# Kernel optimization log

Hardware: AMD Instinct MI355X
Metric: run time of the kernel (lower is better)

## Reference

```python
import jax, jax.numpy as jnp
import numpy as np

FEA, DK, H = 768, 64, 12
B, L = 4, 1024
MASK_VAL = -2**15 + 1  # matches torch masked_fill constant


def setup_inputs() -> dict:
    key = jax.random.key(0)
    ks = jax.random.split(key, 16)
    d = {
        'qx': jax.random.normal(ks[0], (B, L, FEA), jnp.float32),
        'kx': jax.random.normal(ks[1], (B, L, FEA), jnp.float32),
        'vx': jax.random.normal(ks[2], (B, L, FEA), jnp.float32),
        'preScores': jax.random.normal(ks[3], (B, H, L, L), jnp.float32),
        'maskPAD': jax.random.randint(ks[4], (B, L, L), 0, 2, jnp.int32),
    }
    s = 1.0 / np.sqrt(FEA)
    d['WQ_w'] = jax.random.normal(ks[5], (H * DK, FEA), jnp.float32) * s
    d['WQ_b'] = jnp.zeros((H * DK,), jnp.float32)
    d['WK_w'] = jax.random.normal(ks[6], (H * DK, FEA), jnp.float32) * s
    d['WK_b'] = jnp.zeros((H * DK,), jnp.float32)
    d['WV_w'] = jax.random.normal(ks[7], (H * DK, FEA), jnp.float32) * s
    d['WV_b'] = jnp.zeros((H * DK,), jnp.float32)
    d['WO_w'] = jax.random.normal(ks[8], (FEA, H * DK), jnp.float32) * s
    d['WO_b'] = jnp.zeros((FEA,), jnp.float32)
    return d


def reference(qx, kx, vx, preScores, maskPAD,
              WQ_w, WQ_b, WK_w, WK_b, WV_w, WV_b, WO_w, WO_b):
    b, l, c = qx.shape
    # projections -> (B, H, L, dk)
    q = (qx @ WQ_w.T + WQ_b).reshape(b, l, H, DK).transpose(0, 2, 1, 3)
    k = (kx @ WK_w.T + WK_b).reshape(b, l, H, DK).transpose(0, 2, 1, 3)
    v = (vx @ WV_w.T + WV_b).reshape(b, l, H, DK).transpose(0, 2, 1, 3)
    scores = jnp.einsum('bhqd,bhkd->bhqk', q, k) / np.sqrt(DK)
    scores = scores + preScores  # RealFormer residual scores
    scores = jnp.where((maskPAD == 0)[:, None, :, :], jnp.float32(MASK_VAL), scores)
    alpha = jax.nn.softmax(scores, axis=3)  # dropout p=0 (eval/deterministic)
    z = jnp.einsum('bhqk,bhkd->bhqd', alpha, v)
    z = z.transpose(0, 2, 1, 3).reshape(b, l, H * DK)
    z = z @ WO_w.T + WO_b
    return z, scores
```

## Files before the change

### kernel.cpp

```cpp
#include <hip/hip_runtime.h>
#include <hip/hip_bf16.h>

#define B_ 4
#define L_ 1024
#define H_ 12
#define DK_ 64
#define FEA_ 768
#define MASKV (-32767.0f)

typedef __attribute__((ext_vector_type(8))) short bf16x8;
typedef __attribute__((ext_vector_type(4))) short s16x4;
typedef __attribute__((ext_vector_type(4))) float f32x4;
typedef unsigned int u32;

__device__ inline short f2bf(float x) {
  __hip_bfloat16 h = __float2bfloat16(x);
  return __builtin_bit_cast(short, h);
}

#define SZX  (4 * 1024 * 768)
#define SZW  (768 * 768)

__global__ __launch_bounds__(256) void k_cvt(
    const float* __restrict__ qx, const float* __restrict__ kx,
    const float* __restrict__ vx,
    const float* __restrict__ Wq, const float* __restrict__ Wk,
    const float* __restrict__ Wv,
    unsigned short* __restrict__ dst)
{
  const size_t SZX4 = SZX / 4, SZW4 = SZW / 4;
  const size_t total4 = 3 * SZX4 + 3 * SZW4;
  for (size_t i4 = (size_t)blockIdx.x * 256 + threadIdx.x; i4 < total4;
       i4 += (size_t)gridDim.x * 256) {
    const float* src; size_t o4; size_t db;
    if (i4 < SZX4)               { src = qx; o4 = i4;               db = 0; }
    else if (i4 < 2 * SZX4)      { src = kx; o4 = i4 - SZX4;        db = (size_t)SZX; }
    else if (i4 < 3 * SZX4)      { src = vx; o4 = i4 - 2 * SZX4;    db = 2 * (size_t)SZX; }
    else if (i4 < 3 * SZX4 + SZW4)     { src = Wq; o4 = i4 - 3 * SZX4;            db = 3 * (size_t)SZX; }
    else if (i4 < 3 * SZX4 + 2 * SZW4) { src = Wk; o4 = i4 - 3 * SZX4 - SZW4;     db = 3 * (size_t)SZX + SZW; }
    else                               { src = Wv; o4 = i4 - 3 * SZX4 - 2 * SZW4; db = 3 * (size_t)SZX + 2 * (size_t)SZW; }
    float4 v = ((const float4*)src)[o4];
    s16x4 r = {f2bf(v.x), f2bf(v.y), f2bf(v.z), f2bf(v.w)};
    *(s16x4*)(dst + db + o4 * 4) = r;
  }
}

__global__ __launch_bounds__(256) void k_cvt2(
    const float* __restrict__ Wo, unsigned short* __restrict__ dst)
{
  size_t i4 = (size_t)blockIdx.x * 256 + threadIdx.x;
  if (i4 < (size_t)SZW / 4) {
    float4 v = ((const float4*)Wo)[i4];
    s16x4 r = {f2bf(v.x), f2bf(v.y), f2bf(v.z), f2bf(v.w)};
    *(s16x4*)(dst + i4 * 4) = r;
  }
}

__global__ __launch_bounds__(256) void k_proj(
    const unsigned short* __restrict__ qxb, const unsigned short* __restrict__ kxb,
    const unsigned short* __restrict__ vxb,
    const unsigned short* __restrict__ Wqb, const unsigned short* __restrict__ Wkb,
    const unsigned short* __restrict__ Wvb,
    const float* __restrict__ bq, const float* __restrict__ bk,
    const float* __restrict__ bv,
    unsigned short* __restrict__ Qb, unsigned short* __restrict__ Kb,
    unsigned short* __restrict__ Vt)
{
  __shared__ short lA[2][64 * 64];
  __shared__ short lB[2][64 * 64];

  const int which = blockIdx.z;
  const unsigned short* __restrict__ Ab = (which == 0) ? qxb : (which == 1) ? kxb : vxb;
  const unsigned short* __restrict__ Wb = (which == 0) ? Wqb : (which == 1) ? Wkb : Wvb;
  const float* __restrict__ bias = (which == 0) ? bq : (which == 1) ? bk : bv;

  const int tid = threadIdx.x;
  const int lane = tid & 63;
  const int wid = tid >> 6;
  const int wr = wid >> 1, wc = wid & 1;
  const int m0 = blockIdx.x * 64;
  const int n0 = blockIdx.y * 64;
  const int g = lane >> 4, qc = lane & 15;
  const int srow = lane >> 3;
  const int spos = lane & 7;

#define PSTAGE(buf, ktof)                                                      \
  {                                                                            \
    _Pragma("unroll")                                                          \
    for (int i_ = 0; i_ < 2; i_++) {                                           \
      int r0_ = wid * 16 + i_ * 8;                                             \
      int row_ = r0_ + srow;                                                   \
      int cs_ = spos ^ (row_ & 7);                                             \
      __builtin_amdgcn_global_load_lds(                                        \
          (const __attribute__((address_space(1))) u32*)(Ab +                  \
              (size_t)(m0 + row_) * FEA_ + (ktof) + cs_ * 8),                  \
          (__attribute__((address_space(3))) u32*)&lA[buf][r0_ * 64],          \
          16, 0, 0);                                                           \
      __builtin_amdgcn_global_load_lds(                                        \
          (const __attribute__((address_space(1))) u32*)(Wb +                  \
              (size_t)(n0 + row_) * FEA_ + (ktof) + cs_ * 8),                  \
          (__attribute__((address_space(3))) u32*)&lB[buf][r0_ * 64],          \
          16, 0, 0);                                                           \
    }                                                                          \
  }

  f32x4 acc[2][2];
#pragma unroll
  for (int i = 0; i < 2; i++)
#pragma unroll
    for (int j = 0; j < 2; j++) acc[i][j] = f32x4{0.f, 0.f, 0.f, 0.f};

  PSTAGE(0, 0);
  asm volatile("s_waitcnt vmcnt(0)" ::: "memory");
  __builtin_amdgcn_s_barrier();

  for (int kt = 0; kt < 12; kt++) {
    const int cur = kt & 1, nxt = cur ^ 1;
    if (kt < 11) PSTAGE(nxt, (kt + 1) * 64);
    __builtin_amdgcn_sched_barrier(0);
    __builtin_amdgcn_s_setprio(1);
#pragma unroll
    for (int s = 0; s < 2; s++) {
      bf16x8 af[2], bfr[2];
#pragma unroll
      for (int i = 0; i < 2; i++) {
        int ar = wr * 32 + i * 16 + qc;
        af[i] = *(const bf16x8*)&lA[cur][ar * 64 + (((s * 4 + g) ^ (ar & 7)) << 3)];
        int br = wc * 32 + i * 16 + qc;
        bfr[i] = *(const bf16x8*)&lB[cur][br * 64 + (((s * 4 + g) ^ (br & 7)) << 3)];
      }
#pragma unroll
      for (int i = 0; i < 2; i++)
#pragma unroll
        for (int j = 0; j < 2; j++)
          acc[i][j] = __builtin_amdgcn_mfma_f32_16x16x32_bf16(af[i], bfr[j], acc[i][j], 0, 0, 0);
    }
    __builtin_amdgcn_s_setprio(0);
    asm volatile("s_waitcnt vmcnt(0)" ::: "memory");
    __builtin_amdgcn_s_barrier();
  }

  const int cn0 = n0 + wc * 32;
  float bv2[2];
#pragma unroll
  for (int j = 0; j < 2; j++) bv2[j] = bias[cn0 + j * 16 + qc];

#pragma unroll
  for (int i = 0; i < 2; i++) {
    int m = m0 + wr * 32 + i * 16 + g * 4;
    int bb = m >> 10;
    int l = m & 1023;
#pragma unroll
    for (int j = 0; j < 2; j++) {
      int n = cn0 + j * 16 + qc;
      int hh = n >> 6, d = n & 63;
      if (which == 2) {
        s16x4 vv = {f2bf(acc[i][j][0] + bv2[j]), f2bf(acc[i][j][1] + bv2[j]),
                    f2bf(acc[i][j][2] + bv2[j]), f2bf(acc[i][j][3] + bv2[j])};
        *(s16x4*)&Vt[(((size_t)bb * H_ + hh) * DK_ + d) * L_ + l] = vv;
      } else {
#pragma unroll
        for (int r = 0; r < 4; r++) {
          unsigned short v = (unsigned short)f2bf(acc[i][j][r] + bv2[j]);
          if (which == 0) {
            Qb[(((size_t)bb * H_ + hh) * L_ + (l + r)) * DK_ + d] = v;
          } else {
            Kb[(((size_t)bb * H_ + hh) * L_ + (l + r)) * DK_ + d] = v;
          }
        }
      }
    }
  }
#undef PSTAGE
}

__global__ __launch_bounds__(256, 3) void k_attn(
    const unsigned short* __restrict__ Qb, const unsigned short* __restrict__ Kb,
    const unsigned short* __restrict__ Vt,
    const float* __restrict__ preScores, const int* __restrict__ maskPAD,
    float* __restrict__ scoresOut, unsigned short* __restrict__ zp)
{
  __shared__ short lK[2][64 * 64];
  __shared__ short lV[2][64 * 64];
  __shared__ float lU[4][1120];

  const int tid = threadIdx.x, lane = tid & 63, wid = tid >> 6;
  const int bi = blockIdx.x;
  const int slot = bi >> 3;
  const int bh_i = (bi & 7) * 6 + (slot >> 4);
  const int qt = slot & 15;
  const int b = bh_i / H_;
  const int h = bh_i % H_;
  const int q0 = qt * 64;
  const int g = lane >> 4, qr = lane & 15;
  const int qrow = q0 + wid * 16 + qr;
  const int rhi = lane >> 4, klo = lane & 15;
  const int rowCg = q0 + wid * 16 + rhi;

  const size_t bh = (size_t)b * H_ + h;
  const unsigned short* __restrict__ Kbh = Kb + bh * L_ * DK_;
  const unsigned short* __restrict__ Vbh = Vt + bh * DK_ * L_;

  float* lSw = &lU[wid][0];
  short* lPw = (short*)&lU[wid][0];
  float* lLw = &lU[wid][1088];

  const int srow = lane >> 3;
  const int spos = lane & 7;

#define STAGE_KV(buf, kv0)                                                     \
  {                                                                            \
    _Pragma("unroll")                                                          \
    for (int i_ = 0; i_ < 2; i_++) {                                           \
      int r0_ = wid * 16 + i_ * 8;                                             \
      int row_ = r0_ + srow;                                                   \
      int cs_ = spos ^ (row_ & 7);                                             \
      __builtin_amdgcn_global_load_lds(                                        \
          (const __attribute__((address_space(1))) u32*)(Kbh +                 \
              (size_t)((kv0) + row_) * DK_ + cs_ * 8),                         \
          (__attribute__((address_space(3))) u32*)&lK[buf][r0_ * 64],          \
          16, 0, 0);                                                           \
      __builtin_amdgcn_global_load_lds(                                        \
          (const __attribute__((address_space(1))) u32*)(Vbh +                 \
              (size_t)row_ * L_ + (kv0) + cs_ * 8),                            \
          (__attribute__((address_space(3))) u32*)&lV[buf][r0_ * 64],          \
          16, 0, 0);                                                           \
    }                                                                          \
  }

  bf16x8 qf[2];
#pragma unroll
  for (int s = 0; s < 2; s++)
    qf[s] = *(const bf16x8*)(Qb + (bh * L_ + qrow) * DK_ + s * 32 + g * 8);

  f32x4 o[4];
#pragma unroll
  for (int i = 0; i < 4; i++) o[i] = f32x4{0.f, 0.f, 0.f, 0.f};
  float psum[4] = {0.f, 0.f, 0.f, 0.f};

  const size_t psCbase = (bh * L_ + rowCg) * L_ + klo * 4;
  const size_t mkCbase = ((size_t)b * L_ + rowCg) * L_ + klo * 4;

  STAGE_KV(0, 0);
  __builtin_amdgcn_sched_barrier(0);
  float4 psn[4];
  int4 mkn[4];
#pragma unroll
  for (int j = 0; j < 4; j++) {
    psn[j] = *(const float4*)(preScores + psCbase + j * 4096);
    mkn[j] = *(const int4*)(maskPAD + mkCbase + j * 4096);
  }
  asm volatile("s_waitcnt vmcnt(8)" ::: "memory");
  __builtin_amdgcn_s_barrier();

  for (int kt = 0; kt < 16; kt++) {
    const int kv0 = kt * 64;
    const int cur = kt & 1, nxt = cur ^ 1;

    if (kt < 15) {
      STAGE_KV(nxt, kv0 + 64);
    }
    __builtin_amdgcn_sched_barrier(0);

    float4 psc[4]; int4 mkc[4];
#pragma unroll
    for (int j = 0; j < 4; j++) { psc[j] = psn[j]; mkc[j] = mkn[j]; }
    if (kt < 15) {
#pragma unroll
      for (int j = 0; j < 4; j++) {
        psn[j] = *(const float4*)(preScores + psCbase + kv0 + 64 + j * 4096);
        mkn[j] = *(const int4*)(maskPAD + mkCbase + kv0 + 64 + j * 4096);
      }
    }

    f32x4 st[4];
#pragma unroll
    for (int i = 0; i < 4; i++) st[i] = f32x4{0.f, 0.f, 0.f, 0.f};
    __builtin_amdgcn_s_setprio(1);
#pragma unroll
    for (int s = 0; s < 2; s++) {
#pragma unroll
      for (int i = 0; i < 4; i++) {
        int kr = i * 16 + qr;
        bf16x8 kf = *(const bf16x8*)&lK[cur][kr * 64 + (((s * 4 + g) ^ (kr & 7)) << 3)];
        st[i] = __builtin_amdgcn_mfma_f32_16x16x32_bf16(kf, qf[s], st[i], 0, 0, 0);
      }
    }
    __builtin_amdgcn_s_setprio(0);

#pragma unroll
    for (int i = 0; i < 4; i++)
      *(f32x4*)&lSw[qr * 68 + i * 16 + g * 4] = st[i];
    f32x4 stc[4];
#pragma unroll
    for (int j = 0; j < 4; j++)
      stc[j] = *(const f32x4*)&lSw[(4 * j + rhi) * 68 + klo * 4];

#pragma unroll
    for (int j = 0; j < 4; j++) {
      float4 sv;
      sv.x = (mkc[j].x == 0) ? MASKV : stc[j][0] * 0.125f + psc[j].x;
      sv.y = (mkc[j].y == 0) ? MASKV : stc[j][1] * 0.125f + psc[j].y;
      sv.z = (mkc[j].z == 0) ? MASKV : stc[j][2] * 0.125f + psc[j].z;
      sv.w = (mkc[j].w == 0) ? MASKV : stc[j][3] * 0.125f + psc[j].w;
      *(float4*)(scoresOut + psCbase + kv0 + j * 4096) = sv;
      float p0 = __expf(sv.x);
      float p1 = __expf(sv.y);
      float p2 = __expf(sv.z);
      float p3 = __expf(sv.w);
      psum[j] += (p0 + p1) + (p2 + p3);
      s16x4 pw = {f2bf(p0), f2bf(p1), f2bf(p2), f2bf(p3)};
      int rL = 4 * j + rhi;
      int c = klo >> 1, sub = (klo & 1) * 4;
      *(s16x4*)&lPw[rL * 64 + ((c ^ (rL & 7)) << 3) + sub] = pw;
    }

    __builtin_amdgcn_s_setprio(1);
#pragma unroll
    for (int s = 0; s < 2; s++) {
      bf16x8 pf = *(const bf16x8*)&lPw[qr * 64 + (((s * 4 + g) ^ (qr & 7)) << 3)];
#pragma unroll
      for (int i = 0; i < 4; i++) {
        int vr = i * 16 + qr;
        bf16x8 vf = *(const bf16x8*)&lV[cur][vr * 64 + (((s * 4 + g) ^ (vr & 7)) << 3)];
        o[i] = __builtin_amdgcn_mfma_f32_16x16x32_bf16(vf, pf, o[i], 0, 0, 0);
      }
    }
    __builtin_amdgcn_s_setprio(0);

    asm volatile("s_waitcnt vmcnt(12)" ::: "memory");
    __builtin_amdgcn_s_barrier();
  }

#pragma unroll
  for (int j = 0; j < 4; j++) {
    float v = psum[j];
    v += __shfl_xor(v, 1);
    v += __shfl_xor(v, 2);
    v += __shfl_xor(v, 4);
    v += __shfl_xor(v, 8);
    if (klo == 0) lLw[4 * j + rhi] = v;
  }
  float inv = 1.f / lLw[qr];
  size_t zr = ((size_t)b * L_ + qrow) * FEA_ + (size_t)h * DK_;
#pragma unroll
  for (int i = 0; i < 4; i++) {
    s16x4 zw = {f2bf(o[i][0] * inv), f2bf(o[i][1] * inv),
                f2bf(o[i][2] * inv), f2bf(o[i][3] * inv)};
    *(s16x4*)((unsigned short*)zp + zr + i * 16 + g * 4) = zw;
  }
#undef STAGE_KV
}

__global__ __launch_bounds__(256) void k_oproj(
    const unsigned short* __restrict__ zp,
    const unsigned short* __restrict__ Wob, const float* __restrict__ bo,
    float* __restrict__ out)
{
  __shared__ short lA[2][64 * 64];
  __shared__ short lB[2][64 * 64];

  const int tid = threadIdx.x;
  const int lane = tid & 63;
  const int wid = tid >> 6;
  const int wr = wid >> 1, wc = wid & 1;
  const int m0 = blockIdx.x * 64;
  const int n0 = blockIdx.y * 64;
  const int g = lane >> 4, qc = lane & 15;
  const int srow = lane >> 3;
  const int spos = lane & 7;

#define OSTAGE(buf, ktof)                                                      \
  {                                                                            \
    _Pragma("unroll")                                                          \
    for (int i_ = 0; i_ < 2; i_++) {                                           \
      int r0_ = wid * 16 + i_ * 8;                                             \
      int row_ = r0_ + srow;                                                   \
      int cs_ = spos ^ (row_ & 7);                                             \
      __builtin_amdgcn_global_load_lds(                                        \
          (const __attribute__((address_space(1))) u32*)(zp +                  \
              (size_t)(m0 + row_) * FEA_ + (ktof) + cs_ * 8),                  \
          (__attribute__((address_space(3))) u32*)&lA[buf][r0_ * 64],          \
          16, 0, 0);                                                           \
      __builtin_amdgcn_global_load_lds(                                        \
          (const __attribute__((address_space(1))) u32*)(Wob +                 \
              (size_t)(n0 + row_) * FEA_ + (ktof) + cs_ * 8),                  \
          (__attribute__((address_space(3))) u32*)&lB[buf][r0_ * 64],          \
          16, 0, 0);                                                           \
    }                                                                          \
  }

  f32x4 acc[2][2];
#pragma unroll
  for (int i = 0; i < 2; i++)
#pragma unroll
    for (int j = 0; j < 2; j++) acc[i][j] = f32x4{0.f, 0.f, 0.f, 0.f};

  OSTAGE(0, 0);
  asm volatile("s_waitcnt vmcnt(0)" ::: "memory");
  __builtin_amdgcn_s_barrier();

  for (int kt = 0; kt < 12; kt++) {
    const int cur = kt & 1, nxt = cur ^ 1;
    if (kt < 11) OSTAGE(nxt, (kt + 1) * 64);
    __builtin_amdgcn_sched_barrier(0);
    __builtin_amdgcn_s_setprio(1);
#pragma unroll
    for (int s = 0; s < 2; s++) {
      bf16x8 af[2], bfr[2];
#pragma unroll
      for (int i = 0; i < 2; i++) {
        int ar = wr * 32 + i * 16 + qc;
        af[i] = *(const bf16x8*)&lA[cur][ar * 64 + (((s * 4 + g) ^ (ar & 7)) << 3)];
        int br = wc * 32 + i * 16 + qc;
        bfr[i] = *(const bf16x8*)&lB[cur][br * 64 + (((s * 4 + g) ^ (br & 7)) << 3)];
      }
#pragma unroll
      for (int i = 0; i < 2; i++)
#pragma unroll
        for (int j = 0; j < 2; j++)
          acc[i][j] = __builtin_amdgcn_mfma_f32_16x16x32_bf16(af[i], bfr[j], acc[i][j], 0, 0, 0);
    }
    __builtin_amdgcn_s_setprio(0);
    asm volatile("s_waitcnt vmcnt(0)" ::: "memory");
    __builtin_amdgcn_s_barrier();
  }

  const int cn0 = n0 + wc * 32;
  float bv2[2];
#pragma unroll
  for (int j = 0; j < 2; j++) bv2[j] = bo[cn0 + j * 16 + qc];

#pragma unroll
  for (int i = 0; i < 2; i++) {
    int m = m0 + wr * 32 + i * 16 + g * 4;
#pragma unroll
    for (int j = 0; j < 2; j++) {
      int n = cn0 + j * 16 + qc;
#pragma unroll
      for (int r = 0; r < 4; r++) {
        out[(size_t)(m + r) * FEA_ + n] = acc[i][j][r] + bv2[j];
      }
    }
  }
#undef OSTAGE
}

extern "C" void kernel_launch(void* const* d_in, const int* in_sizes, int n_in,
                              void* d_out, int out_size, void* d_ws, size_t ws_size,
                              hipStream_t stream) {
  const float* qx = (const float*)d_in[0];
  const float* kx = (const float*)d_in[1];
  const float* vx = (const float*)d_in[2];
  const float* preScores = (const float*)d_in[3];
  const int* maskPAD = (const int*)d_in[4];
  const float* Wq = (const float*)d_in[5];
  const float* bq = (const float*)d_in[6];
  const float* Wk = (const float*)d_in[7];
  const float* bk = (const float*)d_in[8];
  const float* Wv = (const float*)d_in[9];
  const float* bv = (const float*)d_in[10];
  const float* Wo = (const float*)d_in[11];
  const float* bo = (const float*)d_in[12];

  float* z_out = (float*)d_out;
  float* scores_out = z_out + (size_t)B_ * L_ * FEA_;

  unsigned short* Qb = (unsigned short*)d_ws;
  unsigned short* Kb = Qb + (size_t)B_ * H_ * L_ * DK_;
  unsigned short* Vt = Kb + (size_t)B_ * H_ * L_ * DK_;
  unsigned short* zp = Vt + (size_t)B_ * H_ * L_ * DK_;

  unsigned short* cvtb = (unsigned short*)(scores_out + (50331648 - 5603328));
  const unsigned short* qxb = cvtb;
  const unsigned short* kxb = cvtb + (size_t)SZX;
  const unsigned short* vxb = cvtb + 2 * (size_t)SZX;
  const unsigned short* Wqb = cvtb + 3 * (size_t)SZX;
  const unsigned short* Wkb = cvtb + 3 * (size_t)SZX + (size_t)SZW;
  const unsigned short* Wvb = cvtb + 3 * (size_t)SZX + 2 * (size_t)SZW;

  unsigned short* Wob = Qb;

  k_cvt<<<dim3(1024), 256, 0, stream>>>(qx, kx, vx, Wq, Wk, Wv, cvtb);
  k_proj<<<dim3(64, 12, 3), 256, 0, stream>>>(qxb, kxb, vxb, Wqb, Wkb, Wvb,
                                              bq, bk, bv, Qb, Kb, Vt);
  k_attn<<<dim3(8 * 6 * 16, 1, 1), 256, 0, stream>>>(Qb, Kb, Vt, preScores,
                                                     maskPAD, scores_out, zp);
  k_cvt2<<<dim3(576), 256, 0, stream>>>(Wo, Wob);
  k_oproj<<<dim3(64, 12), 256, 0, stream>>>(zp, Wob, bo, z_out);
}
```

Measured before the change: 156.0 us.

## Pack int32 padding mask into bitmask once and read bits in attention

The conversion kernel now ballots the int32 maskPAD into a 64-bit-per-64-elements bitmask, stored temporarily in the z output buffer. The attention kernel reads a 32-bit word per lane and extracts a 4-bit nibble instead of loading int4 vectors. Each head then reads a mask far smaller than the 16 MB int32 mask, which was re-read for all 12 heads. The cost is one extra pass over the mask in the conversion kernel and scratch space in z_out that k_oproj later overwrites.

```diff
diff --git a/kernel.cpp b/kernel.cpp
--- a/kernel.cpp
+++ b/kernel.cpp
@@ -12,6 +12,7 @@
 typedef __attribute__((ext_vector_type(4))) short s16x4;
 typedef __attribute__((ext_vector_type(4))) float f32x4;
 typedef unsigned int u32;
+typedef unsigned long long u64;
 
 __device__ inline short f2bf(float x) {
   __hip_bfloat16 h = __float2bfloat16(x);
@@ -26,7 +27,8 @@
     const float* __restrict__ vx,
     const float* __restrict__ Wq, const float* __restrict__ Wk,
     const float* __restrict__ Wv,
-    unsigned short* __restrict__ dst)
+    const int* __restrict__ maskPAD,
+    unsigned short* __restrict__ dst, u64* __restrict__ maskPk)
 {
   const size_t SZX4 = SZX / 4, SZW4 = SZW / 4;
   const size_t total4 = 3 * SZX4 + 3 * SZW4;
@@ -42,6 +44,16 @@
     float4 v = ((const float4*)src)[o4];
     s16x4 r = {f2bf(v.x), f2bf(v.y), f2bf(v.z), f2bf(v.w)};
     *(s16x4*)(dst + db + o4 * 4) = r;
+  }
+
+  const size_t NM = (size_t)B_ * L_ * L_;
+  const size_t wgid = ((size_t)blockIdx.x * 256 + threadIdx.x) >> 6;
+  const size_t nwaves = ((size_t)gridDim.x * 256) >> 6;
+  const int ln = threadIdx.x & 63;
+  for (size_t base = wgid * 64; base < NM; base += nwaves * 64) {
+    int m = maskPAD[base + ln];
+    u64 bits = __ballot(m != 0);
+    if (ln == 0) maskPk[base >> 6] = bits;
   }
 }
 
@@ -177,7 +189,7 @@
 __global__ __launch_bounds__(256, 3) void k_attn(
     const unsigned short* __restrict__ Qb, const unsigned short* __restrict__ Kb,
     const unsigned short* __restrict__ Vt,
-    const float* __restrict__ preScores, const int* __restrict__ maskPAD,
+    const float* __restrict__ preScores, const u32* __restrict__ maskPk,
     float* __restrict__ scoresOut, unsigned short* __restrict__ zp)
 {
   __shared__ short lK[2][64 * 64];
@@ -239,16 +251,17 @@
   float psum[4] = {0.f, 0.f, 0.f, 0.f};
 
   const size_t psCbase = (bh * L_ + rowCg) * L_ + klo * 4;
-  const size_t mkCbase = ((size_t)b * L_ + rowCg) * L_ + klo * 4;
+  const size_t mkPbase = (((size_t)b * L_ + rowCg) * 16) * 2 + (klo >> 3);
+  const int mshift = (klo & 7) * 4;
 
   STAGE_KV(0, 0);
   __builtin_amdgcn_sched_barrier(0);
   float4 psn[4];
-  int4 mkn[4];
+  u32 mkn[4];
 #pragma unroll
   for (int j = 0; j < 4; j++) {
     psn[j] = *(const float4*)(preScores + psCbase + j * 4096);
-    mkn[j] = *(const int4*)(maskPAD + mkCbase + j * 4096);
+    mkn[j] = maskPk[mkPbase + j * 128];
   }
   asm volatile("s_waitcnt vmcnt(8)" ::: "memory");
   __builtin_amdgcn_s_barrier();
@@ -262,14 +275,14 @@
     }
     __builtin_amdgcn_sched_barrier(0);
 
-    float4 psc[4]; int4 mkc[4];
+    float4 psc[4]; u32 mkc[4];
 #pragma unroll
     for (int j = 0; j < 4; j++) { psc[j] = psn[j]; mkc[j] = mkn[j]; }
     if (kt < 15) {
 #pragma unroll
       for (int j = 0; j < 4; j++) {
         psn[j] = *(const float4*)(preScores + psCbase + kv0 + 64 + j * 4096);
-        mkn[j] = *(const int4*)(maskPAD + mkCbase + kv0 + 64 + j * 4096);
+        mkn[j] = maskPk[mkPbase + (kt + 1) * 2 + j * 128];
       }
     }
 
@@ -298,11 +311,12 @@
 
 #pragma unroll
     for (int j = 0; j < 4; j++) {
+      u32 nib = (mkc[j] >> mshift) & 0xFu;
       float4 sv;
-      sv.x = (mkc[j].x == 0) ? MASKV : stc[j][0] * 0.125f + psc[j].x;
-      sv.y = (mkc[j].y == 0) ? MASKV : stc[j][1] * 0.125f + psc[j].y;
-      sv.z = (mkc[j].z == 0) ? MASKV : stc[j][2] * 0.125f + psc[j].z;
-      sv.w = (mkc[j].w == 0) ? MASKV : stc[j][3] * 0.125f + psc[j].w;
+      sv.x = ((nib & 1u) == 0) ? MASKV : stc[j][0] * 0.125f + psc[j].x;
+      sv.y = ((nib & 2u) == 0) ? MASKV : stc[j][1] * 0.125f + psc[j].y;
+      sv.z = ((nib & 4u) == 0) ? MASKV : stc[j][2] * 0.125f + psc[j].z;
+      sv.w = ((nib & 8u) == 0) ? MASKV : stc[j][3] * 0.125f + psc[j].w;
       *(float4*)(scoresOut + psCbase + kv0 + j * 4096) = sv;
       float p0 = __expf(sv.x);
       float p1 = __expf(sv.y);
@@ -479,13 +493,17 @@
   const unsigned short* Wkb = cvtb + 3 * (size_t)SZX + (size_t)SZW;
   const unsigned short* Wvb = cvtb + 3 * (size_t)SZX + 2 * (size_t)SZW;
 
+  u64* maskPk = (u64*)z_out;
+
   unsigned short* Wob = Qb;
 
-  k_cvt<<<dim3(1024), 256, 0, stream>>>(qx, kx, vx, Wq, Wk, Wv, cvtb);
+  k_cvt<<<dim3(1024), 256, 0, stream>>>(qx, kx, vx, Wq, Wk, Wv, maskPAD,
+                                        cvtb, maskPk);
   k_proj<<<dim3(64, 12, 3), 256, 0, stream>>>(qxb, kxb, vxb, Wqb, Wkb, Wvb,
                                               bq, bk, bv, Qb, Kb, Vt);
   k_attn<<<dim3(8 * 6 * 16, 1, 1), 256, 0, stream>>>(Qb, Kb, Vt, preScores,
-                                                     maskPAD, scores_out, zp);
+                                                     (const u32*)maskPk,
+                                                     scores_out, zp);
   k_cvt2<<<dim3(576), 256, 0, stream>>>(Wo, Wob);
   k_oproj<<<dim3(64, 12), 256, 0, stream>>>(zp, Wob, bo, z_out);
 }
```

Result: slower. 162.6 us (+4.2%).
